# Performance work log

Measured on AMD Instinct MI355X. Metric: run time of the kernel, lower is better.

The kernel has to match this reference:

```python
import jax, jax.numpy as jnp
import numpy as np

B, S, D, K = 8, 2048, 1024, 204  # K = int(0.1 * seq_len)
LN_EPS = 1e-12


def setup_inputs() -> dict:
    key = jax.random.key(0)
    ks = jax.random.split(key, 8)
    scale = 0.02
    return {
        "input_tensor": jax.random.normal(ks[0], (B, S, D), jnp.float32),
        "attention_mask": jnp.zeros((B, 1, 1, S), jnp.float32),  # unused by module
        "Wq": jax.random.normal(ks[1], (D, K), jnp.float32) * scale,
        "bq": jnp.zeros((K,), jnp.float32),
        "Wk": jax.random.normal(ks[2], (D, K), jnp.float32) * scale,
        "bk": jnp.zeros((K,), jnp.float32),
        "Wv": jax.random.normal(ks[3], (D, D), jnp.float32) * scale,
        "bv": jnp.zeros((D,), jnp.float32),
        "Wd": jax.random.normal(ks[4], (D, D), jnp.float32) * scale,
        "bd": jnp.zeros((D,), jnp.float32),
        "gamma": jnp.ones((D,), jnp.float32),
        "beta": jnp.zeros((D,), jnp.float32),
    }


def reference(input_tensor, attention_mask, Wq, bq, Wk, bk, Wv, bv, Wd, bd, gamma, beta):
    # factorized synthesizer: low-rank (k=204) Q/K projections
    q = input_tensor @ Wq + bq          # [B,S,K]
    k = input_tensor @ Wk + bk          # [B,S,K]
    v = input_tensor @ Wv + bv          # [B,S,D]
    scores = jnp.einsum('bsk,btk->bst', q, k)          # [B,S,S]
    probs = jax.nn.softmax(scores, axis=-1)
    # per-head matmul with broadcast probs == direct matmul on merged heads
    ctx = jnp.einsum('bst,btd->bsd', probs, v)          # [B,S,D]
    h = ctx @ Wd + bd
    y = h + input_tensor                                 # residual
    mean = jnp.mean(y, axis=-1, keepdims=True)
    var = jnp.mean(jnp.square(y - mean), axis=-1, keepdims=True)
    return gamma * (y - mean) / jnp.sqrt(var + LN_EPS) + beta
```

## Files before the change

### kernel.cpp

```cpp
#include <hip/hip_runtime.h>
#include <stdint.h>

#define BB 8
#define SS 2048
#define DD 1024
#define KREAL 204

typedef __attribute__((ext_vector_type(8))) short short8;
typedef __attribute__((ext_vector_type(4))) float floatx4;
typedef uint16_t u16;
typedef uint32_t u32;

__device__ __forceinline__ float bf2f(u16 u) {
    union { float f; u32 i; } c; c.i = ((u32)u) << 16; return c.f;
}
__device__ __forceinline__ u16 f2bf(float f) {
    union { float f; u32 i; } c; c.f = f;
    u32 i = c.i;
    u32 r = (i + 0x7FFFu + ((i >> 16) & 1u)) >> 16;
    return (u16)r;
}

#if defined(__has_builtin)
#if __has_builtin(__builtin_amdgcn_global_load_lds)
#define HAVE_GLL 1
#endif
#endif

__device__ __forceinline__ void gload16(const u16* g, u16* l) {
#ifdef HAVE_GLL
    __builtin_amdgcn_global_load_lds(
        (const __attribute__((address_space(1))) void*)(uintptr_t)g,
        (__attribute__((address_space(3))) void*)(u32)(uintptr_t)(void*)l,
        16, 0, 0);
#else
    *(uint4*)l = *(const uint4*)g;
#endif
}

#define VM_WAIT(N) asm volatile("s_waitcnt vmcnt(" #N ")" ::: "memory")
#define S_BAR()    asm volatile("s_barrier" ::: "memory")

__device__ __forceinline__ void stage64(const u16* __restrict__ src, size_t ld,
                                        u16* lds, int tid) {
#pragma unroll
    for (int j = 0; j < 2; j++) {
        int flat = j * 256 + tid;
        int row = flat >> 3, slot = flat & 7;
        int kg = slot ^ (row & 7);
        gload16(src + (size_t)row * ld + kg * 8, lds + flat * 8);
    }
}
__device__ __forceinline__ short8 frag(const u16* lds, int row, int kslot) {
    return *(const short8*)&lds[(row << 6) + (((kslot ^ (row & 7)) & 7) << 3)];
}

__device__ __forceinline__ short8 frag32(const u16* plane, int row, int ks) {
    return *(const short8*)&plane[(row << 5) + (((ks ^ ((row >> 1) & 3)) & 3) << 3)];
}

template <int MT0, bool LOADB>
__device__ __forceinline__ void phase16(const u16* Apl, const u16* Bpl,
                                        int arow, int brow, int ln, int quad,
                                        short8 (&bv)[4], floatx4 (&acc)[8][4]) {
    short8 af[4];
#pragma unroll
    for (int i = 0; i < 4; i++) af[i] = frag32(Apl, arow + (MT0 + i) * 16 + ln, quad);
    if (LOADB) {
#pragma unroll
        for (int nt = 0; nt < 4; nt++) bv[nt] = frag32(Bpl, brow + nt * 16 + ln, quad);
    }
    __builtin_amdgcn_s_setprio(1);
#pragma unroll
    for (int i = 0; i < 4; i++)
#pragma unroll
        for (int nt = 0; nt < 4; nt++)
            acc[MT0 + i][nt] = __builtin_amdgcn_mfma_f32_16x16x32_bf16(
                af[i], bv[nt], acc[MT0 + i][nt], 0, 0, 0);
    __builtin_amdgcn_s_setprio(0);
}

template <int NT>
__device__ __forceinline__ void gemm_core5(
    const u16* __restrict__ Ag, size_t lda,
    const u16* __restrict__ Bg, size_t ldb,
    u16* lds, int tid, floatx4 (&acc)[8][4]) {
    static_assert(NT >= 3, "ring-5 core needs NT >= 3");
    const int lane = tid & 63, w = tid >> 6;
    const int arow = (w >> 2) * 128, brow = (w & 3) * 64;
    const int ln = lane & 15, quad = lane >> 4;
    const int srow = tid >> 2;
    const int kgp = (tid & 3) ^ ((srow >> 1) & 3);
    const u16* A0 = Ag + (size_t)srow * lda + kgp * 8;
    const u16* A1 = Ag + (size_t)(srow + 128) * lda + kgp * 8;
    const u16* B0 = Bg + (size_t)srow * ldb + kgp * 8;
    const u16* B1 = Bg + (size_t)(srow + 128) * ldb + kgp * 8;
    u16* Al = lds;
    u16* Bl = lds + 5 * 8192;

    auto SH = [&](int sl, int h) {
        size_t koff = (size_t)h * 32;
        gload16(A0 + koff, Al + sl * 8192 + tid * 8);
        gload16(A1 + koff, Al + sl * 8192 + 4096 + tid * 8);
        gload16(B0 + koff, Bl + sl * 8192 + tid * 8);
        gload16(B1 + koff, Bl + sl * 8192 + 4096 + tid * 8);
    };

    SH(0, 0); SH(1, 1); SH(2, 2); SH(3, 3);

    short8 bv[4];
    int sl0 = 0, sl1 = 1;
#pragma unroll 2
    for (int t = 0; t < NT - 2; ++t) {
        const u16* Ap0 = Al + sl0 * 8192;  const u16* Bp0 = Bl + sl0 * 8192;
        const u16* Ap1 = Al + sl1 * 8192;  const u16* Bp1 = Bl + sl1 * 8192;
        const int st = sl0 ? sl0 - 1 : 4;
        VM_WAIT(12); S_BAR();
        SH(st, 2 * t + 4);
        phase16<0, true >(Ap0, Bp0, arow, brow, ln, quad, bv, acc);
        phase16<4, false>(Ap0, Bp0, arow, brow, ln, quad, bv, acc);
        VM_WAIT(12); S_BAR();
        SH(sl0, 2 * t + 5);
        phase16<0, true >(Ap1, Bp1, arow, brow, ln, quad, bv, acc);
        phase16<4, false>(Ap1, Bp1, arow, brow, ln, quad, bv, acc);
        sl0 += 2; if (sl0 >= 5) sl0 -= 5;
        sl1 += 2; if (sl1 >= 5) sl1 -= 5;
    }
    {
        const u16* Ap0 = Al + sl0 * 8192;  const u16* Bp0 = Bl + sl0 * 8192;
        const u16* Ap1 = Al + sl1 * 8192;  const u16* Bp1 = Bl + sl1 * 8192;
        VM_WAIT(12); S_BAR();
        phase16<0, true >(Ap0, Bp0, arow, brow, ln, quad, bv, acc);
        phase16<4, false>(Ap0, Bp0, arow, brow, ln, quad, bv, acc);
        VM_WAIT(8); S_BAR();
        phase16<0, true >(Ap1, Bp1, arow, brow, ln, quad, bv, acc);
        phase16<4, false>(Ap1, Bp1, arow, brow, ln, quad, bv, acc);
        sl0 += 2; if (sl0 >= 5) sl0 -= 5;
        sl1 += 2; if (sl1 >= 5) sl1 -= 5;
    }
    {
        const u16* Ap0 = Al + sl0 * 8192;  const u16* Bp0 = Bl + sl0 * 8192;
        const u16* Ap1 = Al + sl1 * 8192;  const u16* Bp1 = Bl + sl1 * 8192;
        VM_WAIT(4); S_BAR();
        phase16<0, true >(Ap0, Bp0, arow, brow, ln, quad, bv, acc);
        phase16<4, false>(Ap0, Bp0, arow, brow, ln, quad, bv, acc);
        VM_WAIT(0); S_BAR();
        phase16<0, true >(Ap1, Bp1, arow, brow, ln, quad, bv, acc);
        phase16<4, false>(Ap1, Bp1, arow, brow, ln, quad, bv, acc);
    }
}

template <typename F>
__device__ __forceinline__ void store_rm256(u16* smem, u16* gbase, size_t ldc,
                                            int wm, int wn, int ln, int quad,
                                            int tid, F val) {
    for (int half = 0; half < 2; half++) {
        __syncthreads();
        if (wm == half) {
#pragma unroll
            for (int mt = 0; mt < 8; mt++)
#pragma unroll
                for (int nt = 0; nt < 4; nt++)
#pragma unroll
                    for (int r = 0; r < 4; r++)
                        smem[(mt * 16 + quad * 4 + r) * 264 + wn * 64 + nt * 16 + ln] =
                            val(mt, nt, r);
        }
        __syncthreads();
#pragma unroll
        for (int j = 0; j < 8; j++) {
            int flat = j * 512 + tid;
            int row = flat >> 5, c = flat & 31;
            *(uint4*)&gbase[(size_t)(half * 128 + row) * ldc + c * 8] =
                *(const uint4*)&smem[row * 264 + c * 8];
        }
    }
}

template <typename F4>
__device__ __forceinline__ void store_tr256(u16* smem, u16* gbase, size_t ldg,
                                            int wm, int wn, int ln, int quad,
                                            int tid, F4 val4) {
    for (int qr = 0; qr < 4; qr++) {
        __syncthreads();
        if (wn == qr) {
#pragma unroll
            for (int mt = 0; mt < 8; mt++)
#pragma unroll
                for (int nt = 0; nt < 4; nt++) {
                    ushort4 v = val4(mt, nt);
                    *(ushort4*)&smem[(nt * 16 + ln) * 264 + wm * 128 + mt * 16 + quad * 4] = v;
                }
        }
        __syncthreads();
#pragma unroll
        for (int j = 0; j < 4; j++) {
            int flat = j * 512 + tid;
            int c = flat >> 5, r8 = flat & 31;
            *(uint4*)&gbase[(size_t)(qr * 64 + c) * ldg + r8 * 8] =
                *(const uint4*)&smem[c * 264 + r8 * 8];
        }
    }
}

__global__ __launch_bounds__(256) void k_cast_bf16(
    const float* __restrict__ x, u16* __restrict__ o) {
    size_t i = ((size_t)blockIdx.x * 256 + threadIdx.x) * 4;
    float4 v = *(const float4*)&x[i];
    ushort4 p;
    p.x = f2bf(v.x); p.y = f2bf(v.y); p.z = f2bf(v.z); p.w = f2bf(v.w);
    *(ushort4*)&o[i] = p;
}

__global__ __launch_bounds__(256) void k_prep(
    const float* __restrict__ Wq, const float* __restrict__ Wk,
    const float* __restrict__ Wv, const float* __restrict__ Wd,
    const float* __restrict__ bv, const float* __restrict__ bd,
    const float* __restrict__ bq, const float* __restrict__ bk,
    u16* __restrict__ Wqkt, u16* __restrict__ Wv16, u16* __restrict__ Wdt,
    float* __restrict__ bc, float* __restrict__ bqk) {
    const int z = blockIdx.z;
    const int t = threadIdx.x;
    if (z == 4) {
        int id = blockIdx.y * 32 + blockIdx.x;
        if (id < 16) {
            __shared__ float red[4][64];
            int n = id * 64 + (t & 63);
            int dc = t >> 6;
            float s = 0.f;
            for (int d = dc * 256; d < dc * 256 + 256; d++)
                s += bv[d] * Wd[(size_t)d * 1024 + n];
            red[dc][t & 63] = s;
            __syncthreads();
            if (dc == 0) bc[n] = bd[n] + red[0][t & 63] + red[1][t & 63] + red[2][t & 63] + red[3][t & 63];
        } else if (id == 16) {
            for (int i = t; i < 512; i += 256) {
                float v = 0.f;
                if (i < KREAL) v = bq[i];
                else if (i >= 256 && i < 256 + KREAL) v = bk[i - 256];
                bqk[i] = v;
            }
        }
        return;
    }
    __shared__ u16 tile[32][33];
    int k0 = blockIdx.x * 32, n0 = blockIdx.y * 32;
    int tx = t & 31, ty = t >> 5;
    if (z == 2) {
        for (int i = ty; i < 32; i += 8) {
            size_t idx = (size_t)(k0 + i) * 1024 + n0 + tx;
            Wv16[idx] = f2bf(Wv[idx]);
        }
        return;
    }
    const float* W; u16* out; int N, Npad, rowoff;
    if (z == 0)      { W = Wq; out = Wqkt; N = KREAL; Npad = 256;  rowoff = 0;   }
    else if (z == 1) { W = Wk; out = Wqkt; N = KREAL; Npad = 256;  rowoff = 256; }
    else             { W = Wd; out = Wdt;  N = 1024;  Npad = 1024; rowoff = 0;   }
    if (n0 >= Npad) return;
    for (int i = ty; i < 32; i += 8) {
        int n = n0 + tx;
        tile[i][tx] = (n < N) ? f2bf(W[(size_t)(k0 + i) * N + n]) : (u16)0;
    }
    __syncthreads();
    for (int i = ty; i < 32; i += 8) {
        int n = n0 + i;
        if (n < Npad) out[(size_t)(rowoff + n) * 1024 + k0 + tx] = tile[tx][i];
    }
}

__global__ __launch_bounds__(256) void k_gemm64(
    const u16* __restrict__ A, const u16* __restrict__ Bt,
    u16* __restrict__ C, int ldc) {
    __shared__ u16 As[64 * 64];
    __shared__ u16 Bs[64 * 64];
    const int tid = threadIdx.x;
    const int m0 = blockIdx.x * 64, n0 = blockIdx.y * 64;
    const int lane = tid & 63, w = tid >> 6;
    const int ln = lane & 15, quad = lane >> 4;

    floatx4 acc[4];
    floatx4 zero = {0.f, 0.f, 0.f, 0.f};
#pragma unroll
    for (int nt = 0; nt < 4; nt++) acc[nt] = zero;

    for (int kt = 0; kt < 16; kt++) {
        __syncthreads();
        stage64(A + (size_t)m0 * 1024 + kt * 64, 1024, As, tid);
        stage64(Bt + (size_t)n0 * 1024 + kt * 64, 1024, Bs, tid);
        __syncthreads();
#pragma unroll
        for (int kk = 0; kk < 2; kk++) {
            short8 av = frag(As, w * 16 + ln, kk * 4 + quad);
#pragma unroll
            for (int nt = 0; nt < 4; nt++) {
                short8 bvf = frag(Bs, nt * 16 + ln, kk * 4 + quad);
                acc[nt] = __builtin_amdgcn_mfma_f32_16x16x32_bf16(av, bvf, acc[nt], 0, 0, 0);
            }
        }
    }
    const int row0 = m0 + w * 16 + quad * 4;
#pragma unroll
    for (int nt = 0; nt < 4; nt++) {
        const int col = n0 + nt * 16 + ln;
        ushort4 pk;
        pk.x = f2bf(acc[nt][0]); pk.y = f2bf(acc[nt][1]);
        pk.z = f2bf(acc[nt][2]); pk.w = f2bf(acc[nt][3]);
        *reinterpret_cast<ushort4*>(&C[(size_t)col * ldc + row0]) = pk;
    }
}

__global__ __launch_bounds__(512, 2) void k_proj2(
    const u16* __restrict__ A, const u16* __restrict__ Wqkt,
    const u16* __restrict__ Wvdt, const float* __restrict__ bqk,
    u16* __restrict__ qkp, u16* __restrict__ ut) {
    __shared__ __align__(16) u16 lds[81920];
    const int tid = threadIdx.x;
    const int m0 = blockIdx.x * 256;
    const int by = blockIdx.y;
    const int lane = tid & 63, w = tid >> 6;
    const int wm = w >> 2, wn = w & 3;
    const int ln = lane & 15, quad = lane >> 4;

    floatx4 acc[8][4];
    floatx4 zero = {0.f, 0.f, 0.f, 0.f};
#pragma unroll
    for (int mt = 0; mt < 8; mt++)
#pragma unroll
        for (int nt = 0; nt < 4; nt++) acc[mt][nt] = zero;

    const u16* Ag = A + (size_t)m0 * 1024;
    const int n0 = (by < 2) ? by * 256 : (by - 2) * 256;
    const u16* Bg = (by < 2) ? (Wqkt + (size_t)n0 * 1024) : (Wvdt + (size_t)n0 * 1024);
    gemm_core5<16>(Ag, 1024, Bg, 1024, lds, tid, acc);

    if (by < 2) {
        float b4[4];
#pragma unroll
        for (int nt = 0; nt < 4; nt++) b4[nt] = bqk[n0 + wn * 64 + nt * 16 + ln];
        store_rm256(lds, qkp + (size_t)m0 * 512 + n0, 512, wm, wn, ln, quad, tid,
            [&](int mt, int nt, int r) -> u16 {
                return f2bf(acc[mt][nt][r] + b4[nt]);
            });
    } else {
        int b = m0 >> 11, s0loc = m0 & 2047;
        store_tr256(lds, ut + ((size_t)b * DD + n0) * SS + s0loc, SS, wm, wn, ln, quad, tid,
            [&](int mt, int nt) -> ushort4 {
                ushort4 pk;
                pk.x = f2bf(acc[mt][nt][0]); pk.y = f2bf(acc[mt][nt][1]);
                pk.z = f2bf(acc[mt][nt][2]); pk.w = f2bf(acc[mt][nt][3]);
                return pk;
            });
    }
}

__global__ __launch_bounds__(512, 2) void k_qk2(
    const u16* __restrict__ qkp, u16* __restrict__ P, float* __restrict__ lg) {
    __shared__ __align__(16) u16 lds[81920];
    const int tid = threadIdx.x;
    const int s0 = blockIdx.x * 256, t0 = blockIdx.y * 256, bb = blockIdx.z;
    const int lane = tid & 63, w = tid >> 6;
    const int wm = w >> 2, wn = w & 3;
    const int ln = lane & 15, quad = lane >> 4;

    floatx4 acc[8][4];
    floatx4 zero = {0.f, 0.f, 0.f, 0.f};
#pragma unroll
    for (int mt = 0; mt < 8; mt++)
#pragma unroll
        for (int nt = 0; nt < 4; nt++) acc[mt][nt] = zero;

    gemm_core5<4>(qkp + ((size_t)bb * SS + s0) * 512, 512,
                  qkp + ((size_t)bb * SS + t0) * 512 + 256, 512, lds, tid, acc);

#pragma unroll
    for (int mt = 0; mt < 8; mt++)
#pragma unroll
        for (int nt = 0; nt < 4; nt++)
#pragma unroll
            for (int r = 0; r < 4; r++)
                acc[mt][nt][r] = __expf(acc[mt][nt][r] - 30.f);

#pragma unroll
    for (int mt = 0; mt < 8; mt++) {
#pragma unroll
        for (int r = 0; r < 4; r++) {
            float rs = acc[mt][0][r] + acc[mt][1][r] + acc[mt][2][r] + acc[mt][3][r];
            rs += __shfl_xor(rs, 1);
            rs += __shfl_xor(rs, 2);
            rs += __shfl_xor(rs, 4);
            rs += __shfl_xor(rs, 8);
            if (ln == 0)
                atomicAdd(&lg[(size_t)bb * SS + s0 + wm * 128 + mt * 16 + quad * 4 + r], rs);
        }
    }

    store_rm256(lds, P + (size_t)bb * SS * SS + (size_t)s0 * SS + t0, SS,
                wm, wn, ln, quad, tid,
        [&](int mt, int nt, int r) -> u16 { return f2bf(acc[mt][nt][r]); });
}

__global__ __launch_bounds__(512, 2) void k_h2(
    const u16* __restrict__ P, const u16* __restrict__ ut,
    const float* __restrict__ lg, const float* __restrict__ bc,
    const float* __restrict__ xres, float* __restrict__ out) {
    __shared__ __align__(16) u16 lds[81920];
    const int tid = threadIdx.x;
    const int s0 = blockIdx.x * 256, d0 = blockIdx.y * 256, bb = blockIdx.z;
    const int lane = tid & 63, w = tid >> 6;
    const int wm = w >> 2;
    const int ln = lane & 15, quad = lane >> 4;

    floatx4 acc[8][4];
    floatx4 zero = {0.f, 0.f, 0.f, 0.f};
#pragma unroll
    for (int mt = 0; mt < 8; mt++)
#pragma unroll
        for (int nt = 0; nt < 4; nt++) acc[mt][nt] = zero;

    gemm_core5<32>(P + ((size_t)bb * SS + s0) * SS, SS,
                   ut + ((size_t)bb * DD + d0) * SS, SS, lds, tid, acc);

    float* smem = (float*)lds;
    float* outb = out + ((size_t)bb * SS + s0) * DD + d0;
    const float* xb = xres + ((size_t)bb * SS + s0) * DD + d0;
    const float* lgb = lg + (size_t)bb * SS + s0;
    const int wn = w & 3;
    for (int c4 = 0; c4 < 4; c4++) {
        __syncthreads();
        if (wm == (c4 >> 1)) {
#pragma unroll
            for (int i = 0; i < 4; i++)
#pragma unroll
                for (int nt = 0; nt < 4; nt++)
#pragma unroll
                    for (int r = 0; r < 4; r++)
                        smem[(i * 16 + quad * 4 + r) * 260 + wn * 64 + nt * 16 + ln] =
                            acc[(c4 & 1) * 4 + i][nt][r];
        }
        __syncthreads();
#pragma unroll
        for (int j = 0; j < 8; j++) {
            int flat = j * 512 + tid;
            int row = flat >> 6, q = flat & 63;
            float iv = 1.f / lgb[c4 * 64 + row];
            float4 a  = *(const float4*)&smem[row * 260 + q * 4];
            float4 b4 = *(const float4*)&bc[d0 + q * 4];
            float4 xr = *(const float4*)&xb[(size_t)(c4 * 64 + row) * DD + q * 4];
            float4 o;
            o.x = a.x * iv + b4.x + xr.x;
            o.y = a.y * iv + b4.y + xr.y;
            o.z = a.z * iv + b4.z + xr.z;
            o.w = a.w * iv + b4.w + xr.w;
            *(float4*)&outb[(size_t)(c4 * 64 + row) * DD + q * 4] = o;
        }
    }
}

__global__ __launch_bounds__(256) void k_ln_f32(
    float* __restrict__ io, const float* __restrict__ gamma,
    const float* __restrict__ beta) {
    const int tid = threadIdx.x;
    const int lane = tid & 63, w = tid >> 6;
    const size_t row = (size_t)blockIdx.x * 4 + w;
    float* rp = io + row * DD;

    float v[16];
#pragma unroll
    for (int j = 0; j < 4; j++) {
        float4 t = *(const float4*)&rp[j * 256 + lane * 4];
        v[j * 4 + 0] = t.x; v[j * 4 + 1] = t.y; v[j * 4 + 2] = t.z; v[j * 4 + 3] = t.w;
    }
    float s = 0.f, sq = 0.f;
#pragma unroll
    for (int i = 0; i < 16; i++) { s += v[i]; sq += v[i] * v[i]; }
#pragma unroll
    for (int msk = 1; msk < 64; msk <<= 1) {
        s  += __shfl_xor(s,  msk, 64);
        sq += __shfl_xor(sq, msk, 64);
    }
    float mean = s * (1.f / 1024.f);
    float var  = sq * (1.f / 1024.f) - mean * mean;
    float rstd = rsqrtf(fmaxf(var, 0.f) + 1e-12f);
#pragma unroll
    for (int j = 0; j < 4; j++) {
        float4 g  = *(const float4*)&gamma[j * 256 + lane * 4];
        float4 bt = *(const float4*)&beta [j * 256 + lane * 4];
        float4 o;
        o.x = g.x * (v[j * 4 + 0] - mean) * rstd + bt.x;
        o.y = g.y * (v[j * 4 + 1] - mean) * rstd + bt.y;
        o.z = g.z * (v[j * 4 + 2] - mean) * rstd + bt.z;
        o.w = g.w * (v[j * 4 + 3] - mean) * rstd + bt.w;
        *(float4*)&rp[j * 256 + lane * 4] = o;
    }
}

extern "C" void kernel_launch(void* const* d_in, const int* in_sizes, int n_in,
                              void* d_out, int out_size, void* d_ws, size_t ws_size,
                              hipStream_t stream) {
    const float* x     = (const float*)d_in[0];
    const float* Wq    = (const float*)d_in[2];
    const float* bq    = (const float*)d_in[3];
    const float* Wk    = (const float*)d_in[4];
    const float* bk    = (const float*)d_in[5];
    const float* Wv    = (const float*)d_in[6];
    const float* bv    = (const float*)d_in[7];
    const float* Wd    = (const float*)d_in[8];
    const float* bd    = (const float*)d_in[9];
    const float* gamma = (const float*)d_in[10];
    const float* beta  = (const float*)d_in[11];
    float* out = (float*)d_out;

    char* ws = (char*)d_ws;
    u16*   qkp  = (u16*)(ws + 0);
    u16*   ut   = (u16*)(ws + 16777216);
    u16*   P    = (u16*)(ws + 50331648);
    u16*   x16  = (u16*)(ws + 50331648);
    u16*   Wv16 = (u16*)(ws + 83886080);
    u16*   Wvdt = (u16*)(ws + 85983232);
    u16*   Wdt  = (u16*)(ws + 88080384);
    u16*   Wqkt = (u16*)(ws + 90177536);
    float* lg   = (float*)(ws + 117440512);
    float* bc   = (float*)(ws + 117506048);
    float* bqk  = (float*)(ws + 117510144);

    k_cast_bf16<<<dim3(16384), dim3(256), 0, stream>>>(x, x16);
    k_prep<<<dim3(32, 32, 5), dim3(256), 0, stream>>>(Wq, Wk, Wv, Wd, bv, bd, bq, bk,
                                                      Wqkt, Wv16, Wdt, bc, bqk);
    k_gemm64<<<dim3(16, 16), dim3(256), 0, stream>>>(Wv16, Wdt, Wvdt, 1024);

    k_proj2<<<dim3(64, 6), dim3(512), 0, stream>>>(x16, Wqkt, Wvdt, bqk, qkp, ut);

    hipMemsetAsync(lg, 0, (size_t)BB * SS * sizeof(float), stream);

    k_qk2<<<dim3(8, 8, 8), dim3(512), 0, stream>>>(qkp, P, lg);
    k_h2 <<<dim3(8, 4, 8), dim3(512), 0, stream>>>(P, ut, lg, bc, x, out);

    k_ln_f32<<<dim3(4096), dim3(256), 0, stream>>>(out, gamma, beta);
}
```

Measured before the change: 358.4 us.

## Store P and transposed V in K-panel-major layout for contiguous GEMM loads

The probability matrix P and the transposed value matrix ut are now written in a panel-major layout: 32-wide K slices, with each panel holding all rows contiguously. The final GEMM gains a new core variant that steps through these panels with a fixed panel stride, so each tile load reads a contiguous 16 KB block instead of 256 rows strided by the full sequence length. The goal is better DRAM, TLB and cache locality for the main attention-times-V GEMM. The cost is scattered 64-byte segments on the store side of the producer kernels, and the ring-buffer loop body is moved into a shared macro.

```diff
diff --git a/kernel.cpp b/kernel.cpp
--- a/kernel.cpp
+++ b/kernel.cpp
@@ -79,6 +79,48 @@
                 af[i], bv[nt], acc[MT0 + i][nt], 0, 0, 0);
     __builtin_amdgcn_s_setprio(0);
 }
+
+#define RING5_BODY(SHCALL)                                                     \
+    short8 bv[4];                                                              \
+    int sl0 = 0, sl1 = 1;                                                      \
+    _Pragma("unroll 2")                                                        \
+    for (int t = 0; t < NT - 2; ++t) {                                         \
+        const u16* Ap0 = Al + sl0 * 8192;  const u16* Bp0 = Bl + sl0 * 8192;   \
+        const u16* Ap1 = Al + sl1 * 8192;  const u16* Bp1 = Bl + sl1 * 8192;   \
+        const int st = sl0 ? sl0 - 1 : 4;                                      \
+        VM_WAIT(12); S_BAR();                                                  \
+        SHCALL(st, 2 * t + 4);                                                 \
+        phase16<0, true >(Ap0, Bp0, arow, brow, ln, quad, bv, acc);            \
+        phase16<4, false>(Ap0, Bp0, arow, brow, ln, quad, bv, acc);            \
+        VM_WAIT(12); S_BAR();                                                  \
+        SHCALL(sl0, 2 * t + 5);                                                \
+        phase16<0, true >(Ap1, Bp1, arow, brow, ln, quad, bv, acc);            \
+        phase16<4, false>(Ap1, Bp1, arow, brow, ln, quad, bv, acc);            \
+        sl0 += 2; if (sl0 >= 5) sl0 -= 5;                                      \
+        sl1 += 2; if (sl1 >= 5) sl1 -= 5;                                      \
+    }                                                                          \
+    {                                                                          \
+        const u16* Ap0 = Al + sl0 * 8192;  const u16* Bp0 = Bl + sl0 * 8192;   \
+        const u16* Ap1 = Al + sl1 * 8192;  const u16* Bp1 = Bl + sl1 * 8192;   \
+        VM_WAIT(12); S_BAR();                                                  \
+        phase16<0, true >(Ap0, Bp0, arow, brow, ln, quad, bv, acc);            \
+        phase16<4, false>(Ap0, Bp0, arow, brow, ln, quad, bv, acc);            \
+        VM_WAIT(8); S_BAR();                                                   \
+        phase16<0, true >(Ap1, Bp1, arow, brow, ln, quad, bv, acc);            \
+        phase16<4, false>(Ap1, Bp1, arow, brow, ln, quad, bv, acc);            \
+        sl0 += 2; if (sl0 >= 5) sl0 -= 5;                                      \
+        sl1 += 2; if (sl1 >= 5) sl1 -= 5;                                      \
+    }                                                                          \
+    {                                                                          \
+        const u16* Ap0 = Al + sl0 * 8192;  const u16* Bp0 = Bl + sl0 * 8192;   \
+        const u16* Ap1 = Al + sl1 * 8192;  const u16* Bp1 = Bl + sl1 * 8192;   \
+        VM_WAIT(4); S_BAR();                                                   \
+        phase16<0, true >(Ap0, Bp0, arow, brow, ln, quad, bv, acc);            \
+        phase16<4, false>(Ap0, Bp0, arow, brow, ln, quad, bv, acc);            \
+        VM_WAIT(0); S_BAR();                                                   \
+        phase16<0, true >(Ap1, Bp1, arow, brow, ln, quad, bv, acc);            \
+        phase16<4, false>(Ap1, Bp1, arow, brow, ln, quad, bv, acc);            \
+    }
 
 template <int NT>
 __device__ __forceinline__ void gemm_core5(
@@ -107,47 +149,36 @@
     };
 
     SH(0, 0); SH(1, 1); SH(2, 2); SH(3, 3);
-
-    short8 bv[4];
-    int sl0 = 0, sl1 = 1;
-#pragma unroll 2
-    for (int t = 0; t < NT - 2; ++t) {
-        const u16* Ap0 = Al + sl0 * 8192;  const u16* Bp0 = Bl + sl0 * 8192;
-        const u16* Ap1 = Al + sl1 * 8192;  const u16* Bp1 = Bl + sl1 * 8192;
-        const int st = sl0 ? sl0 - 1 : 4;
-        VM_WAIT(12); S_BAR();
-        SH(st, 2 * t + 4);
-        phase16<0, true >(Ap0, Bp0, arow, brow, ln, quad, bv, acc);
-        phase16<4, false>(Ap0, Bp0, arow, brow, ln, quad, bv, acc);
-        VM_WAIT(12); S_BAR();
-        SH(sl0, 2 * t + 5);
-        phase16<0, true >(Ap1, Bp1, arow, brow, ln, quad, bv, acc);
-        phase16<4, false>(Ap1, Bp1, arow, brow, ln, quad, bv, acc);
-        sl0 += 2; if (sl0 >= 5) sl0 -= 5;
-        sl1 += 2; if (sl1 >= 5) sl1 -= 5;
-    }
-    {
-        const u16* Ap0 = Al + sl0 * 8192;  const u16* Bp0 = Bl + sl0 * 8192;
-        const u16* Ap1 = Al + sl1 * 8192;  const u16* Bp1 = Bl + sl1 * 8192;
-        VM_WAIT(12); S_BAR();
-        phase16<0, true >(Ap0, Bp0, arow, brow, ln, quad, bv, acc);
-        phase16<4, false>(Ap0, Bp0, arow, brow, ln, quad, bv, acc);
-        VM_WAIT(8); S_BAR();
-        phase16<0, true >(Ap1, Bp1, arow, brow, ln, quad, bv, acc);
-        phase16<4, false>(Ap1, Bp1, arow, brow, ln, quad, bv, acc);
-        sl0 += 2; if (sl0 >= 5) sl0 -= 5;
-        sl1 += 2; if (sl1 >= 5) sl1 -= 5;
-    }
-    {
-        const u16* Ap0 = Al + sl0 * 8192;  const u16* Bp0 = Bl + sl0 * 8192;
-        const u16* Ap1 = Al + sl1 * 8192;  const u16* Bp1 = Bl + sl1 * 8192;
-        VM_WAIT(4); S_BAR();
-        phase16<0, true >(Ap0, Bp0, arow, brow, ln, quad, bv, acc);
-        phase16<4, false>(Ap0, Bp0, arow, brow, ln, quad, bv, acc);
-        VM_WAIT(0); S_BAR();
-        phase16<0, true >(Ap1, Bp1, arow, brow, ln, quad, bv, acc);
-        phase16<4, false>(Ap1, Bp1, arow, brow, ln, quad, bv, acc);
-    }
+    RING5_BODY(SH)
+}
+
+template <int NT>
+__device__ __forceinline__ void gemm_core5p(
+    const u16* __restrict__ Ag, size_t PSA,
+    const u16* __restrict__ Bg, size_t PSB,
+    u16* lds, int tid, floatx4 (&acc)[8][4]) {
+    static_assert(NT >= 3, "ring-5 core needs NT >= 3");
+    const int lane = tid & 63, w = tid >> 6;
+    const int arow = (w >> 2) * 128, brow = (w & 3) * 64;
+    const int ln = lane & 15, quad = lane >> 4;
+    const int srow = tid >> 2;
+    const int kgp = (tid & 3) ^ ((srow >> 1) & 3);
+    const u16* A0 = Ag + (size_t)srow * 32 + kgp * 8;
+    const u16* A1 = A0 + 4096;
+    const u16* B0 = Bg + (size_t)srow * 32 + kgp * 8;
+    const u16* B1 = B0 + 4096;
+    u16* Al = lds;
+    u16* Bl = lds + 5 * 8192;
+
+    auto SH = [&](int sl, int h) {
+        gload16(A0 + (size_t)h * PSA, Al + sl * 8192 + tid * 8);
+        gload16(A1 + (size_t)h * PSA, Al + sl * 8192 + 4096 + tid * 8);
+        gload16(B0 + (size_t)h * PSB, Bl + sl * 8192 + tid * 8);
+        gload16(B1 + (size_t)h * PSB, Bl + sl * 8192 + 4096 + tid * 8);
+    };
+
+    SH(0, 0); SH(1, 1); SH(2, 2); SH(3, 3);
+    RING5_BODY(SH)
 }
 
 template <typename F>
@@ -177,10 +208,38 @@
     }
 }
 
+template <typename F>
+__device__ __forceinline__ void store_pm256(u16* smem, u16* pb, int s0, int t0,
+                                            int wm, int wn, int ln, int quad,
+                                            int tid, F val) {
+    for (int half = 0; half < 2; half++) {
+        __syncthreads();
+        if (wm == half) {
+#pragma unroll
+            for (int mt = 0; mt < 8; mt++)
+#pragma unroll
+                for (int nt = 0; nt < 4; nt++)
+#pragma unroll
+                    for (int r = 0; r < 4; r++)
+                        smem[(mt * 16 + quad * 4 + r) * 264 + wn * 64 + nt * 16 + ln] =
+                            val(mt, nt, r);
+        }
+        __syncthreads();
+#pragma unroll
+        for (int j = 0; j < 8; j++) {
+            int flat = j * 512 + tid;
+            int row = flat >> 5, c = flat & 31;
+            size_t panel = (size_t)(t0 >> 5) + (c >> 2);
+            *(uint4*)&pb[panel * 65536 + (size_t)(s0 + half * 128 + row) * 32 + (c & 3) * 8] =
+                *(const uint4*)&smem[row * 264 + c * 8];
+        }
+    }
+}
+
 template <typename F4>
-__device__ __forceinline__ void store_tr256(u16* smem, u16* gbase, size_t ldg,
-                                            int wm, int wn, int ln, int quad,
-                                            int tid, F4 val4) {
+__device__ __forceinline__ void store_tr256_pm(u16* smem, u16* utb, int n0,
+                                               int s0loc, int wm, int wn,
+                                               int ln, int quad, int tid, F4 val4) {
     for (int qr = 0; qr < 4; qr++) {
         __syncthreads();
         if (wn == qr) {
@@ -197,7 +256,8 @@
         for (int j = 0; j < 4; j++) {
             int flat = j * 512 + tid;
             int c = flat >> 5, r8 = flat & 31;
-            *(uint4*)&gbase[(size_t)(qr * 64 + c) * ldg + r8 * 8] =
+            size_t panel = (size_t)(s0loc >> 5) + (r8 >> 2);
+            *(uint4*)&utb[panel * 32768 + (size_t)(n0 + qr * 64 + c) * 32 + (r8 & 3) * 8] =
                 *(const uint4*)&smem[c * 264 + r8 * 8];
         }
     }
@@ -344,7 +404,7 @@
             });
     } else {
         int b = m0 >> 11, s0loc = m0 & 2047;
-        store_tr256(lds, ut + ((size_t)b * DD + n0) * SS + s0loc, SS, wm, wn, ln, quad, tid,
+        store_tr256_pm(lds, ut + (size_t)b * DD * SS, n0, s0loc, wm, wn, ln, quad, tid,
             [&](int mt, int nt) -> ushort4 {
                 ushort4 pk;
                 pk.x = f2bf(acc[mt][nt][0]); pk.y = f2bf(acc[mt][nt][1]);
@@ -395,8 +455,7 @@
         }
     }
 
-    store_rm256(lds, P + (size_t)bb * SS * SS + (size_t)s0 * SS + t0, SS,
-                wm, wn, ln, quad, tid,
+    store_pm256(lds, P + (size_t)bb * SS * SS, s0, t0, wm, wn, ln, quad, tid,
         [&](int mt, int nt, int r) -> u16 { return f2bf(acc[mt][nt][r]); });
 }
 
@@ -418,8 +477,9 @@
 #pragma unroll
         for (int nt = 0; nt < 4; nt++) acc[mt][nt] = zero;
 
-    gemm_core5<32>(P + ((size_t)bb * SS + s0) * SS, SS,
-                   ut + ((size_t)bb * DD + d0) * SS, SS, lds, tid, acc);
+    gemm_core5p<32>(P + (size_t)bb * SS * SS + (size_t)s0 * 32, (size_t)SS * 32,
+                    ut + (size_t)bb * DD * SS + (size_t)d0 * 32, (size_t)DD * 32,
+                    lds, tid, acc);
 
     float* smem = (float*)lds;
     float* outb = out + ((size_t)bb * SS + s0) * DD + d0;
```

New measurement: 367.0 us. 2.4% more time.
